# Performance work log

Hardware: AMD Instinct MI355X
Metric: run time of the kernel (lower is better)

## Reference

```python
import jax, jax.numpy as jnp
import numpy as np

N_NODES = 100000
N_EDGES = 3200000
D_IN, D_HID, D_OUT = 256, 256, 256
B, V, C = 64, 50, 64
DEC_H1, DEC_H2, N_CLS = 512, 256, 1000
NEG_INF = -1e9


def setup_inputs() -> dict:
    key = jax.random.key(0)
    ks = jax.random.split(key, 20)
    s = lambda d: 1.0 / np.sqrt(d)
    return {
        'edge_index': jax.random.randint(ks[0], (2, N_EDGES), 0, N_NODES, dtype=jnp.int64 if jax.config.jax_enable_x64 else jnp.int32),
        'edge_weight': jax.random.uniform(ks[1], (N_EDGES,), dtype=jnp.float32),
        'codes_x': jax.random.randint(ks[2], (B, V, C), 0, N_NODES, dtype=jnp.int64 if jax.config.jax_enable_x64 else jnp.int32),
        'node_emb': jax.random.normal(ks[3], (N_NODES, D_IN), jnp.float32) * 0.02,
        'W1': jax.random.normal(ks[4], (D_IN, D_HID), jnp.float32) * s(D_IN),
        'b1': jnp.zeros((D_HID,), jnp.float32),
        'W2': jax.random.normal(ks[5], (D_HID, D_OUT), jnp.float32) * s(D_HID),
        'b2': jnp.zeros((D_OUT,), jnp.float32),
        'Wv': jax.random.normal(ks[6], (D_OUT, D_OUT), jnp.float32) * s(D_OUT),
        'uv': jax.random.normal(ks[7], (D_OUT,), jnp.float32) * s(D_OUT),
        'Wp': jax.random.normal(ks[8], (D_OUT, D_OUT), jnp.float32) * s(D_OUT),
        'up': jax.random.normal(ks[9], (D_OUT,), jnp.float32) * s(D_OUT),
        'Wd1': jax.random.normal(ks[10], (D_OUT, DEC_H1), jnp.float32) * s(D_OUT),
        'bd1': jnp.zeros((DEC_H1,), jnp.float32),
        'Wd2': jax.random.normal(ks[11], (DEC_H1, DEC_H2), jnp.float32) * s(DEC_H1),
        'bd2': jnp.zeros((DEC_H2,), jnp.float32),
        'Wd3': jax.random.normal(ks[12], (DEC_H2, N_CLS), jnp.float32) * s(DEC_H2),
        'bd3': jnp.zeros((N_CLS,), jnp.float32),
    }


def reference(edge_index, edge_weight, codes_x, node_emb, W1, b1, W2, b2,
              Wv, uv, Wp, up, Wd1, bd1, Wd2, bd2, Wd3, bd3):
    n = node_emb.shape[0]
    src, dst = edge_index[0], edge_index[1]

    def agg(x):  # weighted message passing: out_i = sum_{e: dst=i} w_e * x[src_e]
        return jax.ops.segment_sum(x[src] * edge_weight[:, None], dst, num_segments=n)

    # 2-layer weighted GCN over the code ontology graph (dropout in eval mode)
    h = jax.nn.relu(agg(node_emb) @ W1 + b1)          # [N, D_hid]
    emb = agg(h) @ W2 + b2                             # [N, D_out]

    # Ragged per-visit code attention, vectorized with masks (code id 0 = padding)
    code_mask = codes_x > 0                            # [B, V, C]
    ce = emb[codes_x]                                  # [B, V, C, D]
    ev = jnp.tanh(jnp.einsum('bvcd,de->bvce', ce, Wv)) @ uv   # [B, V, C]
    av = jax.nn.softmax(jnp.where(code_mask, ev, NEG_INF), axis=-1)
    vemb = jnp.einsum('bvc,bvcd->bvd', av, ce)         # [B, V, D]
    visit_mask = code_mask.any(-1)                     # [B, V]
    vemb = jnp.where(visit_mask[..., None], vemb, 0.0)

    # Per-patient visit attention over valid visits only
    ep = jnp.tanh(vemb @ Wp) @ up                      # [B, V]
    ap = jax.nn.softmax(jnp.where(visit_mask, ep, NEG_INF), axis=-1)
    pemb = jnp.einsum('bv,bvd->bd', ap, vemb)          # [B, D]
    pemb = jnp.where(visit_mask.any(-1)[:, None], pemb, 0.0)  # empty patient -> zeros

    # Decoder MLP classifier (train_type='direct')
    h1 = jax.nn.relu(pemb @ Wd1 + bd1)
    h2 = jax.nn.relu(h1 @ Wd2 + bd2)
    return h2 @ Wd3 + bd3                              # [B, n_classes]
```

## Files before the change

kernel.cpp:

```cpp
#include <hip/hip_runtime.h>
#include <hip/hip_bf16.h>
#include <math.h>


#define D 256
#define BPAT 64
#define VIS 50
#define CODES 64
#define NEG_INF -1e9f
#define MPAD 100096
#define BINB 32
#define NBIN 3125
#define SORTCAP 1536

typedef unsigned short ushort_t;
typedef short short8 __attribute__((ext_vector_type(8)));
typedef float f32x4 __attribute__((ext_vector_type(4)));

__device__ __forceinline__ float blo(unsigned u) { return __uint_as_float(u << 16); }
__device__ __forceinline__ float bhi(unsigned u) { return __uint_as_float(u & 0xffff0000u); }
__device__ __forceinline__ float bf2f(ushort_t u) { return __uint_as_float((unsigned)u << 16); }
__device__ __forceinline__ ushort_t f2bfu(float f) {
    __hip_bfloat16 h = __float2bfloat16(f);
    return *reinterpret_cast<ushort_t*>(&h);
}
__device__ __forceinline__ unsigned pack2(float a, float b) {
    return (unsigned)f2bfu(a) | ((unsigned)f2bfu(b) << 16);
}


__global__ __launch_bounds__(512) void bin_count_kernel(
    const int* __restrict__ ei, int* __restrict__ bincount, int ne) {
    __shared__ int h[NBIN];
    for (int i = threadIdx.x; i < NBIN; i += 512) h[i] = 0;
    __syncthreads();
    int stride = gridDim.x * 512;
    for (int e = blockIdx.x * 512 + threadIdx.x; e < ne; e += stride)
        atomicAdd(&h[ei[(size_t)ne + e] >> 5], 1);
    __syncthreads();
    for (int i = threadIdx.x; i < NBIN; i += 512) {
        int c = h[i];
        if (c) atomicAdd(&bincount[i], c);
    }
}

__global__ __launch_bounds__(64) void bin_scan_kernel(
    const int* __restrict__ bincount, int* __restrict__ binstart,
    int* __restrict__ bincursor, int* __restrict__ rp, int ne, int nn) {
    __shared__ int carry;
    int lane = threadIdx.x;
    if (lane == 0) carry = 0;
    __syncthreads();
    for (int base = 0; base < NBIN; base += 64) {
        int i = base + lane;
        int v = (i < NBIN) ? bincount[i] : 0;
        int x = v;
        #pragma unroll
        for (int d = 1; d < 64; d <<= 1) {
            int y = __shfl_up(x, (unsigned)d, 64);
            if (lane >= d) x += y;
        }
        int c = carry;
        if (i < NBIN) { int ex = c + x - v; binstart[i] = ex; bincursor[i] = ex; }
        __syncthreads();
        if (lane == 63) carry = c + x;
        __syncthreads();
    }
    if (lane == 0) { binstart[NBIN] = ne; rp[nn] = ne; }
}

__global__ __launch_bounds__(512) void partition_kernel(
    const int* __restrict__ ei, const float* __restrict__ ew,
    int* __restrict__ bincursor, uint2* __restrict__ ptmp, int ne) {
    __shared__ int h[NBIN];
    __shared__ int base_[NBIN];
    for (int i = threadIdx.x; i < NBIN; i += 512) h[i] = 0;
    __syncthreads();
    int stride = gridDim.x * 512;
    for (int e = blockIdx.x * 512 + threadIdx.x; e < ne; e += stride)
        atomicAdd(&h[ei[(size_t)ne + e] >> 5], 1);
    __syncthreads();
    for (int i = threadIdx.x; i < NBIN; i += 512) {
        int c = h[i];
        base_[i] = c ? atomicAdd(&bincursor[i], c) : 0;
        h[i] = 0;
    }
    __syncthreads();
    for (int e = blockIdx.x * 512 + threadIdx.x; e < ne; e += stride) {
        int dd = ei[(size_t)ne + e];
        int ss = ei[e];
        float w = ew[e];
        int bin = dd >> 5;
        int r = atomicAdd(&h[bin], 1);
        ptmp[base_[bin] + r] =
            make_uint2((unsigned)ss | ((unsigned)(dd & 31) << 17),
                       __float_as_uint(w));
    }
}

__global__ __launch_bounds__(256) void binsort_kernel(
    const uint2* __restrict__ ptmp, const int* __restrict__ binstart,
    uint2* __restrict__ epair, int* __restrict__ rp) {
    int b = blockIdx.x;
    int tid = threadIdx.x;
    int beg = binstart[b], end = binstart[b + 1];
    int nE = end - beg;
    __shared__ uint2 sbuf[SORTCAP];
    __shared__ int cnt[BINB];
    __shared__ int cur[BINB];
    if (tid < BINB) cnt[tid] = 0;
    __syncthreads();
    if (nE <= SORTCAP) {
        for (int i = tid; i < nE; i += 256) {
            uint2 p = ptmp[beg + i];
            sbuf[i] = p;
            atomicAdd(&cnt[(p.x >> 17) & 31], 1);
        }
        __syncthreads();
        if (tid < BINB) {
            int v = cnt[tid];
            int x = v;
            #pragma unroll
            for (int d = 1; d < BINB; d <<= 1) {
                int y = __shfl_up(x, (unsigned)d, BINB);
                if (tid >= d) x += y;
            }
            int start = beg + x - v;
            cur[tid] = start;
            rp[b * BINB + tid] = start;
        }
        __syncthreads();
        for (int i = tid; i < nE; i += 256) {
            uint2 p = sbuf[i];
            int dl = (p.x >> 17) & 31;
            int pos = atomicAdd(&cur[dl], 1);
            epair[pos] = make_uint2(p.x & 0x1FFFF, p.y);
        }
    } else {
        for (int i = beg + tid; i < end; i += 256)
            atomicAdd(&cnt[(ptmp[i].x >> 17) & 31], 1);
        __syncthreads();
        if (tid < BINB) {
            int v = cnt[tid];
            int x = v;
            #pragma unroll
            for (int d = 1; d < BINB; d <<= 1) {
                int y = __shfl_up(x, (unsigned)d, BINB);
                if (tid >= d) x += y;
            }
            int start = beg + x - v;
            cur[tid] = start;
            rp[b * BINB + tid] = start;
        }
        __syncthreads();
        for (int i = beg + tid; i < end; i += 256) {
            uint2 p = ptmp[i];
            int dl = (p.x >> 17) & 31;
            int pos = atomicAdd(&cur[dl], 1);
            epair[pos] = make_uint2(p.x & 0x1FFFF, p.y);
        }
    }
}

__global__ __launch_bounds__(256) void transpose_w4_kernel(
    const float* __restrict__ Wa, const float* __restrict__ Wb,
    const float* __restrict__ Wc, const float* __restrict__ Wd,
    ushort_t* __restrict__ Ta, ushort_t* __restrict__ Tb,
    ushort_t* __restrict__ Tc, ushort_t* __restrict__ Td) {
    const float* W;
    ushort_t* Wt;
    switch (blockIdx.z) {
        case 0: W = Wa; Wt = Ta; break;
        case 1: W = Wb; Wt = Tb; break;
        case 2: W = Wc; Wt = Tc; break;
        default: W = Wd; Wt = Td; break;
    }
    __shared__ float t[32][33];
    int bx = blockIdx.x * 32;
    int by = blockIdx.y * 32;
    int lx = threadIdx.x & 31, ly = threadIdx.x >> 5;
    #pragma unroll
    for (int i = 0; i < 32; i += 8)
        t[ly + i][lx] = W[(size_t)(by + ly + i) * 256 + bx + lx];
    __syncthreads();
    #pragma unroll
    for (int i = 0; i < 32; i += 8)
        Wt[(size_t)(bx + ly + i) * 256 + by + lx] = f2bfu(t[lx][ly + i]);
}

__device__ __forceinline__ void acc8(float* a, uint4 v, float w) {
    a[0] += w * blo(v.x); a[1] += w * bhi(v.x);
    a[2] += w * blo(v.y); a[3] += w * bhi(v.y);
    a[4] += w * blo(v.z); a[5] += w * bhi(v.z);
    a[6] += w * blo(v.w); a[7] += w * bhi(v.w);
}

template<int ACT>
__global__ __launch_bounds__(256) void agg_bf16_kernel(
    const ushort_t* __restrict__ x, const int* __restrict__ rp,
    const uint2* __restrict__ ep, const float* __restrict__ bias,
    ushort_t* __restrict__ out, int n) {
    int wv = (int)(((size_t)blockIdx.x * blockDim.x + threadIdx.x) >> 6);
    int lane = threadIdx.x & 63;
    if (wv >= n) return;
    int half = lane >> 5;
    int l32 = lane & 31;
    int beg = rp[wv], end = rp[wv + 1];
    float a[8] = {};
    int e = beg;
    for (; e + 16 <= end; e += 16) {
        uint2 p0 = ep[e + half];
        uint2 p1 = ep[e + 2 + half];
        uint2 p2 = ep[e + 4 + half];
        uint2 p3 = ep[e + 6 + half];
        uint2 p4 = ep[e + 8 + half];
        uint2 p5 = ep[e + 10 + half];
        uint2 p6 = ep[e + 12 + half];
        uint2 p7 = ep[e + 14 + half];
        uint4 v0 = ((const uint4*)(x + (size_t)p0.x * D))[l32];
        uint4 v1 = ((const uint4*)(x + (size_t)p1.x * D))[l32];
        uint4 v2 = ((const uint4*)(x + (size_t)p2.x * D))[l32];
        uint4 v3 = ((const uint4*)(x + (size_t)p3.x * D))[l32];
        uint4 v4 = ((const uint4*)(x + (size_t)p4.x * D))[l32];
        uint4 v5 = ((const uint4*)(x + (size_t)p5.x * D))[l32];
        uint4 v6 = ((const uint4*)(x + (size_t)p6.x * D))[l32];
        uint4 v7 = ((const uint4*)(x + (size_t)p7.x * D))[l32];
        acc8(a, v0, __uint_as_float(p0.y));
        acc8(a, v1, __uint_as_float(p1.y));
        acc8(a, v2, __uint_as_float(p2.y));
        acc8(a, v3, __uint_as_float(p3.y));
        acc8(a, v4, __uint_as_float(p4.y));
        acc8(a, v5, __uint_as_float(p5.y));
        acc8(a, v6, __uint_as_float(p6.y));
        acc8(a, v7, __uint_as_float(p7.y));
    }
    for (; e + 4 <= end; e += 4) {
        uint2 p0 = ep[e + half];
        uint2 p1 = ep[e + 2 + half];
        uint4 v0 = ((const uint4*)(x + (size_t)p0.x * D))[l32];
        uint4 v1 = ((const uint4*)(x + (size_t)p1.x * D))[l32];
        acc8(a, v0, __uint_as_float(p0.y));
        acc8(a, v1, __uint_as_float(p1.y));
    }
    for (; e + 2 <= end; e += 2) {
        uint2 p0 = ep[e + half];
        uint4 v0 = ((const uint4*)(x + (size_t)p0.x * D))[l32];
        acc8(a, v0, __uint_as_float(p0.y));
    }
    if (e < end) {
        uint2 p0 = ep[e];
        uint4 v0 = ((const uint4*)(x + (size_t)p0.x * D))[l32];
        acc8(a, v0, half ? 0.f : __uint_as_float(p0.y));
    }
    #pragma unroll
    for (int j = 0; j < 8; ++j) a[j] += __shfl_xor(a[j], 32, 64);
    if (half == 0) {
        float4 b0 = ((const float4*)bias)[l32 * 2];
        float4 b1 = ((const float4*)bias)[l32 * 2 + 1];
        a[0] += b0.x; a[1] += b0.y; a[2] += b0.z; a[3] += b0.w;
        a[4] += b1.x; a[5] += b1.y; a[6] += b1.z; a[7] += b1.w;
        if (ACT == 1) {
            #pragma unroll
            for (int j = 0; j < 8; ++j) a[j] = fmaxf(a[j], 0.f);
        }
        uint4 o;
        o.x = pack2(a[0], a[1]); o.y = pack2(a[2], a[3]);
        o.z = pack2(a[4], a[5]); o.w = pack2(a[6], a[7]);
        ((uint4*)(out + (size_t)wv * D))[l32] = o;
    }
}

__global__ __launch_bounds__(512) void gemm_f32a_kernel(
    const float* __restrict__ Af, const ushort_t* __restrict__ Wt,
    ushort_t* __restrict__ out, int nvalid) {
    __shared__ __align__(16) ushort_t As[128 * 32];
    __shared__ __align__(16) ushort_t Bs[256 * 32];
    const int tid = threadIdx.x;
    const int lane = tid & 63;
    const int wv = tid >> 6;
    const int wr = wv >> 2, wc = wv & 3;
    const size_t brow = (size_t)blockIdx.x * 128;

    const int ra = tid >> 2, ca = tid & 3;
    const int rb1 = ra + 128;
    const int csa = ca ^ ((ra >> 1) & 3);
    const int arow = (int)brow + ra;
    const bool aval = arow < nvalid;
    const float* gAf = Af + (size_t)arow * 256 + ca * 8;
    const ushort_t* gB0 = Wt + (size_t)ra  * 256 + ca * 8;
    const ushort_t* gB1 = Wt + (size_t)rb1 * 256 + ca * 8;
    ushort_t* lA  = As + ra * 32 + csa * 8;
    ushort_t* lB0 = Bs + ra * 32 + csa * 8;
    ushort_t* lB1 = Bs + rb1 * 32 + csa * 8;

    const int g = lane >> 4, rl = lane & 15;
    int aoff[4], boff[4];
    #pragma unroll
    for (int m = 0; m < 4; ++m) {
        int row = wr * 64 + m * 16 + rl;
        aoff[m] = row * 32 + (g ^ ((row >> 1) & 3)) * 8;
    }
    #pragma unroll
    for (int n = 0; n < 4; ++n) {
        int row = wc * 64 + n * 16 + rl;
        boff[n] = row * 32 + (g ^ ((row >> 1) & 3)) * 8;
    }

    f32x4 acc[4][4] = {};
    float4 pa0 = make_float4(0.f, 0.f, 0.f, 0.f), pa1 = pa0;
    if (aval) { pa0 = *(const float4*)gAf; pa1 = *(const float4*)(gAf + 4); }
    uint4 vb0 = *(const uint4*)gB0;
    uint4 vb1 = *(const uint4*)gB1;

    for (int ks = 0; ks < 8; ++ks) {
        uint4 va;
        va.x = pack2(pa0.x, pa0.y); va.y = pack2(pa0.z, pa0.w);
        va.z = pack2(pa1.x, pa1.y); va.w = pack2(pa1.z, pa1.w);
        *(uint4*)lA = va; *(uint4*)lB0 = vb0; *(uint4*)lB1 = vb1;
        __syncthreads();
        if (ks < 7) {
            int k0 = (ks + 1) * 32;
            if (aval) {
                pa0 = *(const float4*)(gAf + k0);
                pa1 = *(const float4*)(gAf + k0 + 4);
            }
            vb0 = *(const uint4*)(gB0 + k0);
            vb1 = *(const uint4*)(gB1 + k0);
        }
        short8 af[4], bfv[4];
        #pragma unroll
        for (int m = 0; m < 4; ++m) af[m] = *(const short8*)(As + aoff[m]);
        #pragma unroll
        for (int n = 0; n < 4; ++n) bfv[n] = *(const short8*)(Bs + boff[n]);
        #pragma unroll
        for (int m = 0; m < 4; ++m)
            #pragma unroll
            for (int n = 0; n < 4; ++n)
                acc[m][n] = __builtin_amdgcn_mfma_f32_16x16x32_bf16(
                    af[m], bfv[n], acc[m][n], 0, 0, 0);
        __syncthreads();
    }

    #pragma unroll
    for (int m = 0; m < 4; ++m) {
        #pragma unroll
        for (int r = 0; r < 4; ++r) {
            size_t row = brow + wr * 64 + m * 16 + g * 4 + r;
            #pragma unroll
            for (int n = 0; n < 4; ++n) {
                int col = wc * 64 + n * 16 + rl;
                out[row * 256 + col] = f2bfu(acc[m][n][r]);
            }
        }
    }
}

template<int MODE>
__global__ __launch_bounds__(512) void mfma_gemm_kernel(
    const ushort_t* __restrict__ A, const ushort_t* __restrict__ Wt,
    const float* __restrict__ bias, ushort_t* __restrict__ out,
    const float* __restrict__ u, float* __restrict__ tout, int mvalid) {
    __shared__ __align__(16) ushort_t As[128 * 32];
    __shared__ __align__(16) ushort_t Bs[256 * 32];
    __shared__ float s_t[128];
    const int tid = threadIdx.x;
    const int lane = tid & 63;
    const int wv = tid >> 6;
    const int wr = wv >> 2, wc = wv & 3;
    const size_t brow = (size_t)blockIdx.x * 128;

    const int ra = tid >> 2, ca = tid & 3;
    const int rb1 = ra + 128;
    const int csa = ca ^ ((ra >> 1) & 3);
    const ushort_t* gA  = A  + (brow + ra) * 256 + ca * 8;
    const ushort_t* gB0 = Wt + (size_t)ra  * 256 + ca * 8;
    const ushort_t* gB1 = Wt + (size_t)rb1 * 256 + ca * 8;
    ushort_t* lA  = As + ra * 32 + csa * 8;
    ushort_t* lB0 = Bs + ra * 32 + csa * 8;
    ushort_t* lB1 = Bs + rb1 * 32 + csa * 8;

    const int g = lane >> 4, rl = lane & 15;
    int aoff[4], boff[4];
    #pragma unroll
    for (int m = 0; m < 4; ++m) {
        int row = wr * 64 + m * 16 + rl;
        aoff[m] = row * 32 + (g ^ ((row >> 1) & 3)) * 8;
    }
    #pragma unroll
    for (int n = 0; n < 4; ++n) {
        int row = wc * 64 + n * 16 + rl;
        boff[n] = row * 32 + (g ^ ((row >> 1) & 3)) * 8;
    }

    if (MODE == 2 && tid < 128) s_t[tid] = 0.f;

    f32x4 acc[4][4] = {};
    uint4 va  = *(const uint4*)gA;
    uint4 vb0 = *(const uint4*)gB0;
    uint4 vb1 = *(const uint4*)gB1;

    for (int ks = 0; ks < 8; ++ks) {
        *(uint4*)lA = va; *(uint4*)lB0 = vb0; *(uint4*)lB1 = vb1;
        __syncthreads();
        if (ks < 7) {
            int k0 = (ks + 1) * 32;
            va  = *(const uint4*)(gA + k0);
            vb0 = *(const uint4*)(gB0 + k0);
            vb1 = *(const uint4*)(gB1 + k0);
        }
        short8 af[4], bfv[4];
        #pragma unroll
        for (int m = 0; m < 4; ++m) af[m] = *(const short8*)(As + aoff[m]);
        #pragma unroll
        for (int n = 0; n < 4; ++n) bfv[n] = *(const short8*)(Bs + boff[n]);
        #pragma unroll
        for (int m = 0; m < 4; ++m)
            #pragma unroll
            for (int n = 0; n < 4; ++n)
                acc[m][n] = __builtin_amdgcn_mfma_f32_16x16x32_bf16(
                    af[m], bfv[n], acc[m][n], 0, 0, 0);
        __syncthreads();
    }

    if (MODE == 2) {
        float uvv[4];
        #pragma unroll
        for (int n = 0; n < 4; ++n) uvv[n] = u[wc * 64 + n * 16 + rl];
        #pragma unroll
        for (int m = 0; m < 4; ++m) {
            #pragma unroll
            for (int r = 0; r < 4; ++r) {
                float v = 0.f;
                #pragma unroll
                for (int n = 0; n < 4; ++n) v += tanhf(acc[m][n][r]) * uvv[n];
                v += __shfl_xor(v, 1, 64);
                v += __shfl_xor(v, 2, 64);
                v += __shfl_xor(v, 4, 64);
                v += __shfl_xor(v, 8, 64);
                if (rl == 0) atomicAdd(&s_t[wr * 64 + m * 16 + g * 4 + r], v);
            }
        }
        __syncthreads();
        if (tid < 128 && brow + tid < (size_t)mvalid) tout[brow + tid] = s_t[tid];
    } else {
        #pragma unroll
        for (int m = 0; m < 4; ++m) {
            #pragma unroll
            for (int r = 0; r < 4; ++r) {
                size_t row = brow + wr * 64 + m * 16 + g * 4 + r;
                #pragma unroll
                for (int n = 0; n < 4; ++n) {
                    int col = wc * 64 + n * 16 + rl;
                    float v = acc[m][n][r] + (bias ? bias[col] : 0.f);
                    out[row * 256 + col] = f2bfu(v);
                }
            }
        }
    }
}

__global__ __launch_bounds__(256) void code_attn_kernel(
    const int* __restrict__ codes, const float* __restrict__ t,
    const ushort_t* __restrict__ emb, ushort_t* __restrict__ vembB,
    int* __restrict__ vmask) {
    int bv = blockIdx.x;
    int tid = threadIdx.x;
    __shared__ int s_codes[CODES];
    __shared__ float s_av[CODES];
    __shared__ int s_valid;
    if (tid < 64) {
        int c = codes[(size_t)bv * CODES + tid];
        s_codes[tid] = c;
        float e = (c > 0) ? t[c] : NEG_INF;
        float m = e;
        #pragma unroll
        for (int d = 32; d; d >>= 1) m = fmaxf(m, __shfl_xor(m, d, 64));
        float ex = expf(e - m);
        float s = ex;
        #pragma unroll
        for (int d = 32; d; d >>= 1) s += __shfl_xor(s, d, 64);
        s_av[tid] = ex / s;
        if (tid == 0) s_valid = (m > -1e8f) ? 1 : 0;
    }
    __syncthreads();
    float acc = 0.f;
    #pragma unroll 4
    for (int c = 0; c < CODES; ++c) {
        int node = s_codes[c];
        if (node > 0) acc += s_av[c] * bf2f(emb[(size_t)node * D + tid]);
    }
    int valid = s_valid;
    vembB[(size_t)bv * D + tid] = f2bfu(valid ? acc : 0.f);
    if (tid == 0) vmask[bv] = valid;
}

__global__ __launch_bounds__(256) void patient_kernel(
    const ushort_t* __restrict__ vembB, const float* __restrict__ epr,
    const int* __restrict__ vmask, float* __restrict__ pemb) {
    int b = blockIdx.x;
    int tid = threadIdx.x;
    __shared__ float s_ap[VIS];
    __shared__ int s_any;
    if (tid < 64) {
        float e = -3e38f;
        if (tid < VIS) e = vmask[b * VIS + tid] ? epr[b * VIS + tid] : NEG_INF;
        float m = e;
        #pragma unroll
        for (int d = 32; d; d >>= 1) m = fmaxf(m, __shfl_xor(m, d, 64));
        float ex = (tid < VIS) ? expf(e - m) : 0.f;
        float s = ex;
        #pragma unroll
        for (int d = 32; d; d >>= 1) s += __shfl_xor(s, d, 64);
        if (tid < VIS) s_ap[tid] = ex / s;
        if (tid == 0) s_any = (m > -1e8f) ? 1 : 0;
    }
    __syncthreads();
    float acc = 0.f;
    for (int v = 0; v < VIS; ++v)
        acc += s_ap[v] * bf2f(vembB[((size_t)b * VIS + v) * D + tid]);
    pemb[b * D + tid] = s_any ? acc : 0.f;
}

__global__ __launch_bounds__(256) void gemm_rowcol(
    const float* __restrict__ A, const float* __restrict__ W,
    const float* __restrict__ bias, float* __restrict__ C,
    int M, int N, int K, int act) {
    int row = blockIdx.x;
    int col = blockIdx.y * 256 + threadIdx.x;
    if (col >= N) return;
    const float* a = A + (size_t)row * K;
    float acc = bias ? bias[col] : 0.f;
    #pragma unroll 4
    for (int k = 0; k < K; ++k) acc = fmaf(a[k], W[(size_t)k * N + col], acc);
    if (act == 1) acc = fmaxf(acc, 0.f);
    C[(size_t)row * N + col] = acc;
}

extern "C" void kernel_launch(void* const* d_in, const int* in_sizes, int n_in,
                              void* d_out, int out_size, void* d_ws, size_t ws_size,
                              hipStream_t stream) {
    const int* edge_index    = (const int*)d_in[0];
    const float* edge_weight = (const float*)d_in[1];
    const int* codes         = (const int*)d_in[2];
    const float* node_emb    = (const float*)d_in[3];
    const float* W1 = (const float*)d_in[4];
    const float* b1 = (const float*)d_in[5];
    const float* W2 = (const float*)d_in[6];
    const float* b2 = (const float*)d_in[7];
    const float* Wv = (const float*)d_in[8];
    const float* uv = (const float*)d_in[9];
    const float* Wp = (const float*)d_in[10];
    const float* up = (const float*)d_in[11];
    const float* Wd1 = (const float*)d_in[12];
    const float* bd1 = (const float*)d_in[13];
    const float* Wd2 = (const float*)d_in[14];
    const float* bd2 = (const float*)d_in[15];
    const float* Wd3 = (const float*)d_in[16];
    const float* bd3 = (const float*)d_in[17];

    const int NE = in_sizes[1];
    const int NN = in_sizes[3] / D;

    char* ws = (char*)d_ws;
    size_t off = 0;
    auto alloc = [&](size_t bytes) -> void* {
        void* p = ws + off;
        off += (bytes + 255) & ~(size_t)255;
        return p;
    };
    ushort_t* zbuf = (ushort_t*)alloc((size_t)MPAD * D * 2);
    ushort_t* hbuf = (ushort_t*)alloc((size_t)MPAD * D * 2);
    ushort_t* embB = (ushort_t*)alloc((size_t)MPAD * D * 2);
    uint2* ptmp   = (uint2*)alloc((size_t)NE * 8);
    uint2* epair  = (uint2*)alloc((size_t)NE * 8);
    int* bincount = (int*)alloc((size_t)NBIN * 4);
    int* binstart = (int*)alloc((size_t)(NBIN + 1) * 4);
    int* bincursor= (int*)alloc((size_t)NBIN * 4);
    int* rp       = (int*)alloc((size_t)(NN + 1) * 4);
    ushort_t* W1t = (ushort_t*)alloc(256 * 256 * 2);
    ushort_t* W2t = (ushort_t*)alloc(256 * 256 * 2);
    ushort_t* Wvt = (ushort_t*)alloc(256 * 256 * 2);
    ushort_t* Wpt = (ushort_t*)alloc(256 * 256 * 2);
    float* tbuf  = (float*)alloc((size_t)NN * 4);
    ushort_t* vembB = (ushort_t*)alloc((size_t)BPAT * VIS * D * 2);
    int*   vmask = (int*)  alloc((size_t)BPAT * VIS * 4);
    float* epr   = (float*)alloc((size_t)BPAT * VIS * 4);
    float* pemb  = (float*)alloc((size_t)BPAT * D * 4);
    float* h1    = (float*)alloc((size_t)BPAT * 512 * 4);
    float* h2    = (float*)alloc((size_t)BPAT * D * 4);
    (void)ws_size; (void)n_in; (void)out_size;

    const int ab = NN / 4;

    hipMemsetAsync(bincount, 0, (size_t)NBIN * 4, stream);
    bin_count_kernel<<<256, 512, 0, stream>>>(edge_index, bincount, NE);
    bin_scan_kernel<<<1, 64, 0, stream>>>(bincount, binstart, bincursor, rp, NE, NN);
    partition_kernel<<<128, 512, 0, stream>>>(edge_index, edge_weight,
                                              bincursor, ptmp, NE);
    binsort_kernel<<<NBIN, 256, 0, stream>>>(ptmp, binstart, epair, rp);

    transpose_w4_kernel<<<dim3(8, 8, 4), 256, 0, stream>>>(
        W1, W2, Wv, Wp, W1t, W2t, Wvt, Wpt);

    gemm_f32a_kernel<<<MPAD / 128, 512, 0, stream>>>(node_emb, W1t, zbuf, NN);
    agg_bf16_kernel<1><<<ab, 256, 0, stream>>>(zbuf, rp, epair, b1, hbuf, NN);

    mfma_gemm_kernel<1><<<MPAD / 128, 512, 0, stream>>>(
        hbuf, W2t, nullptr, zbuf, nullptr, nullptr, 0);
    agg_bf16_kernel<0><<<ab, 256, 0, stream>>>(zbuf, rp, epair, b2, embB, NN);

    mfma_gemm_kernel<2><<<MPAD / 128, 512, 0, stream>>>(
        embB, Wvt, nullptr, nullptr, uv, tbuf, NN);

    code_attn_kernel<<<BPAT * VIS, 256, 0, stream>>>(codes, tbuf, embB, vembB, vmask);

    mfma_gemm_kernel<2><<<BPAT * VIS / 128, 512, 0, stream>>>(
        vembB, Wpt, nullptr, nullptr, up, epr, BPAT * VIS);

    patient_kernel<<<BPAT, 256, 0, stream>>>(vembB, epr, vmask, pemb);
    gemm_rowcol<<<dim3(BPAT, 2), 256, 0, stream>>>(pemb, Wd1, bd1, h1, BPAT, 512, D, 1);
    gemm_rowcol<<<dim3(BPAT, 1), 256, 0, stream>>>(h1, Wd2, bd2, h2, BPAT, D, 512, 1);
    gemm_rowcol<<<dim3(BPAT, 4), 256, 0, stream>>>(h2, Wd3, bd3, (float*)d_out, BPAT, 1000, D, 0);
}
```

Before: 893.9 us.

## Fuse weight transpose into bin count and patient attention with decoder MLP

Merges the weight-transpose kernel into the edge bin-count kernel as extra blocks, and merges patient attention with the three decoder GEMMs into one kernel using shared memory for intermediates. Removes the branch on padding codes in code attention, relying on their zero softmax weight, and doubles the partition kernel grid. The aim is to cut launch overhead and global round-trips, though the fused decoder runs serially within only 64 blocks.

```diff
diff --git a/kernel.cpp b/kernel.cpp
--- a/kernel.cpp
+++ b/kernel.cpp
@@ -28,19 +28,43 @@
     return (unsigned)f2bfu(a) | ((unsigned)f2bfu(b) << 16);
 }
 
-
-__global__ __launch_bounds__(512) void bin_count_kernel(
-    const int* __restrict__ ei, int* __restrict__ bincount, int ne) {
+__global__ __launch_bounds__(512) void count_transpose_kernel(
+    const int* __restrict__ ei, int* __restrict__ bincount, int ne,
+    const float* __restrict__ Wa, const float* __restrict__ Wb,
+    const float* __restrict__ Wc, const float* __restrict__ Wd,
+    ushort_t* __restrict__ Ta, ushort_t* __restrict__ Tb,
+    ushort_t* __restrict__ Tc, ushort_t* __restrict__ Td) {
     __shared__ int h[NBIN];
-    for (int i = threadIdx.x; i < NBIN; i += 512) h[i] = 0;
-    __syncthreads();
-    int stride = gridDim.x * 512;
-    for (int e = blockIdx.x * 512 + threadIdx.x; e < ne; e += stride)
-        atomicAdd(&h[ei[(size_t)ne + e] >> 5], 1);
-    __syncthreads();
-    for (int i = threadIdx.x; i < NBIN; i += 512) {
-        int c = h[i];
-        if (c) atomicAdd(&bincount[i], c);
+    __shared__ float tt[2][32][33];
+    if (blockIdx.x < 256) {
+        for (int i = threadIdx.x; i < NBIN; i += 512) h[i] = 0;
+        __syncthreads();
+        const int stride = 256 * 512;
+        for (int e = blockIdx.x * 512 + threadIdx.x; e < ne; e += stride)
+            atomicAdd(&h[ei[(size_t)ne + e] >> 5], 1);
+        __syncthreads();
+        for (int i = threadIdx.x; i < NBIN; i += 512) {
+            int c = h[i];
+            if (c) atomicAdd(&bincount[i], c);
+        }
+    } else {
+        int tile = (blockIdx.x - 256) * 2 + (threadIdx.x >> 8);
+        int which = tile >> 6, rem = tile & 63;
+        int bx = (rem & 7) << 5, by = (rem >> 3) << 5;
+        const float* W = (which == 0) ? Wa : (which == 1) ? Wb
+                        : (which == 2) ? Wc : Wd;
+        ushort_t* Wt = (which == 0) ? Ta : (which == 1) ? Tb
+                      : (which == 2) ? Tc : Td;
+        int hf = threadIdx.x >> 8;
+        int ltid = threadIdx.x & 255;
+        int lx = ltid & 31, ly = ltid >> 5;
+        #pragma unroll
+        for (int i = 0; i < 32; i += 8)
+            tt[hf][ly + i][lx] = W[(size_t)(by + ly + i) * 256 + bx + lx];
+        __syncthreads();
+        #pragma unroll
+        for (int i = 0; i < 32; i += 8)
+            Wt[(size_t)(bx + ly + i) * 256 + by + lx] = f2bfu(tt[hf][lx][ly + i]);
     }
 }
 
@@ -160,32 +184,6 @@
             epair[pos] = make_uint2(p.x & 0x1FFFF, p.y);
         }
     }
-}
-
-__global__ __launch_bounds__(256) void transpose_w4_kernel(
-    const float* __restrict__ Wa, const float* __restrict__ Wb,
-    const float* __restrict__ Wc, const float* __restrict__ Wd,
-    ushort_t* __restrict__ Ta, ushort_t* __restrict__ Tb,
-    ushort_t* __restrict__ Tc, ushort_t* __restrict__ Td) {
-    const float* W;
-    ushort_t* Wt;
-    switch (blockIdx.z) {
-        case 0: W = Wa; Wt = Ta; break;
-        case 1: W = Wb; Wt = Tb; break;
-        case 2: W = Wc; Wt = Tc; break;
-        default: W = Wd; Wt = Td; break;
-    }
-    __shared__ float t[32][33];
-    int bx = blockIdx.x * 32;
-    int by = blockIdx.y * 32;
-    int lx = threadIdx.x & 31, ly = threadIdx.x >> 5;
-    #pragma unroll
-    for (int i = 0; i < 32; i += 8)
-        t[ly + i][lx] = W[(size_t)(by + ly + i) * 256 + bx + lx];
-    __syncthreads();
-    #pragma unroll
-    for (int i = 0; i < 32; i += 8)
-        Wt[(size_t)(bx + ly + i) * 256 + by + lx] = f2bfu(t[lx][ly + i]);
 }
 
 __device__ __forceinline__ void acc8(float* a, uint4 v, float w) {
@@ -484,23 +482,29 @@
     }
     __syncthreads();
     float acc = 0.f;
-    #pragma unroll 4
-    for (int c = 0; c < CODES; ++c) {
-        int node = s_codes[c];
-        if (node > 0) acc += s_av[c] * bf2f(emb[(size_t)node * D + tid]);
-    }
+    #pragma unroll 8
+    for (int c = 0; c < CODES; ++c)
+        acc += s_av[c] * bf2f(emb[(size_t)s_codes[c] * D + tid]);
     int valid = s_valid;
     vembB[(size_t)bv * D + tid] = f2bfu(valid ? acc : 0.f);
     if (tid == 0) vmask[bv] = valid;
 }
 
-__global__ __launch_bounds__(256) void patient_kernel(
+__global__ __launch_bounds__(512) void patient_dec_kernel(
     const ushort_t* __restrict__ vembB, const float* __restrict__ epr,
-    const int* __restrict__ vmask, float* __restrict__ pemb) {
+    const int* __restrict__ vmask,
+    const float* __restrict__ Wd1, const float* __restrict__ bd1,
+    const float* __restrict__ Wd2, const float* __restrict__ bd2,
+    const float* __restrict__ Wd3, const float* __restrict__ bd3,
+    float* __restrict__ outp) {
     int b = blockIdx.x;
     int tid = threadIdx.x;
     __shared__ float s_ap[VIS];
+    __shared__ float s_x[256];
+    __shared__ float s_h1[512];
+    __shared__ float s_h2[256];
     __shared__ int s_any;
+
     if (tid < 64) {
         float e = -3e38f;
         if (tid < VIS) e = vmask[b * VIS + tid] ? epr[b * VIS + tid] : NEG_INF;
@@ -515,25 +519,36 @@
         if (tid == 0) s_any = (m > -1e8f) ? 1 : 0;
     }
     __syncthreads();
-    float acc = 0.f;
-    for (int v = 0; v < VIS; ++v)
-        acc += s_ap[v] * bf2f(vembB[((size_t)b * VIS + v) * D + tid]);
-    pemb[b * D + tid] = s_any ? acc : 0.f;
-}
-
-__global__ __launch_bounds__(256) void gemm_rowcol(
-    const float* __restrict__ A, const float* __restrict__ W,
-    const float* __restrict__ bias, float* __restrict__ C,
-    int M, int N, int K, int act) {
-    int row = blockIdx.x;
-    int col = blockIdx.y * 256 + threadIdx.x;
-    if (col >= N) return;
-    const float* a = A + (size_t)row * K;
-    float acc = bias ? bias[col] : 0.f;
-    #pragma unroll 4
-    for (int k = 0; k < K; ++k) acc = fmaf(a[k], W[(size_t)k * N + col], acc);
-    if (act == 1) acc = fmaxf(acc, 0.f);
-    C[(size_t)row * N + col] = acc;
+    if (tid < 256) {
+        float acc = 0.f;
+        for (int v = 0; v < VIS; ++v)
+            acc += s_ap[v] * bf2f(vembB[((size_t)b * VIS + v) * D + tid]);
+        s_x[tid] = s_any ? acc : 0.f;
+    }
+    __syncthreads();
+    {
+        float acc = bd1[tid];
+        #pragma unroll 8
+        for (int k = 0; k < 256; ++k)
+            acc = fmaf(s_x[k], Wd1[(size_t)k * 512 + tid], acc);
+        s_h1[tid] = fmaxf(acc, 0.f);
+    }
+    __syncthreads();
+    if (tid < 256) {
+        float acc = bd2[tid];
+        #pragma unroll 8
+        for (int k = 0; k < 512; ++k)
+            acc = fmaf(s_h1[k], Wd2[(size_t)k * 256 + tid], acc);
+        s_h2[tid] = fmaxf(acc, 0.f);
+    }
+    __syncthreads();
+    for (int j = tid; j < 1000; j += 512) {
+        float acc = bd3[j];
+        #pragma unroll 8
+        for (int k = 0; k < 256; ++k)
+            acc = fmaf(s_h2[k], Wd3[(size_t)k * 1000 + j], acc);
+        outp[(size_t)b * 1000 + j] = acc;
+    }
 }
 
 extern "C" void kernel_launch(void* const* d_in, const int* in_sizes, int n_in,
@@ -585,22 +600,17 @@
     ushort_t* vembB = (ushort_t*)alloc((size_t)BPAT * VIS * D * 2);
     int*   vmask = (int*)  alloc((size_t)BPAT * VIS * 4);
     float* epr   = (float*)alloc((size_t)BPAT * VIS * 4);
-    float* pemb  = (float*)alloc((size_t)BPAT * D * 4);
-    float* h1    = (float*)alloc((size_t)BPAT * 512 * 4);
-    float* h2    = (float*)alloc((size_t)BPAT * D * 4);
     (void)ws_size; (void)n_in; (void)out_size;
 
     const int ab = NN / 4;
 
     hipMemsetAsync(bincount, 0, (size_t)NBIN * 4, stream);
-    bin_count_kernel<<<256, 512, 0, stream>>>(edge_index, bincount, NE);
+    count_transpose_kernel<<<256 + 128, 512, 0, stream>>>(
+        edge_index, bincount, NE, W1, W2, Wv, Wp, W1t, W2t, Wvt, Wpt);
     bin_scan_kernel<<<1, 64, 0, stream>>>(bincount, binstart, bincursor, rp, NE, NN);
-    partition_kernel<<<128, 512, 0, stream>>>(edge_index, edge_weight,
+    partition_kernel<<<256, 512, 0, stream>>>(edge_index, edge_weight,
                                               bincursor, ptmp, NE);
     binsort_kernel<<<NBIN, 256, 0, stream>>>(ptmp, binstart, epair, rp);
-
-    transpose_w4_kernel<<<dim3(8, 8, 4), 256, 0, stream>>>(
-        W1, W2, Wv, Wp, W1t, W2t, Wvt, Wpt);
 
     gemm_f32a_kernel<<<MPAD / 128, 512, 0, stream>>>(node_emb, W1t, zbuf, NN);
     agg_bf16_kernel<1><<<ab, 256, 0, stream>>>(zbuf, rp, epair, b1, hbuf, NN);
@@ -617,8 +627,6 @@
     mfma_gemm_kernel<2><<<BPAT * VIS / 128, 512, 0, stream>>>(
         vembB, Wpt, nullptr, nullptr, up, epr, BPAT * VIS);
 
-    patient_kernel<<<BPAT, 256, 0, stream>>>(vembB, epr, vmask, pemb);
-    gemm_rowcol<<<dim3(BPAT, 2), 256, 0, stream>>>(pemb, Wd1, bd1, h1, BPAT, 512, D, 1);
-    gemm_rowcol<<<dim3(BPAT, 1), 256, 0, stream>>>(h1, Wd2, bd2, h2, BPAT, D, 512, 1);
-    gemm_rowcol<<<dim3(BPAT, 4), 256, 0, stream>>>(h2, Wd3, bd3, (float*)d_out, BPAT, 1000, D, 0);
-}
+    patient_dec_kernel<<<BPAT, 512, 0, stream>>>(
+        vembB, epr, vmask, Wd1, bd1, Wd2, bd2, Wd3, bd3, (float*)d_out);
+}
```

Result: faster. 802.7 us (-10.2%).
